# Kernel optimization log

Measured on AMD Instinct MI355X. Metric: run time of the kernel, lower is better.

The kernel has to match this reference:

```python
import jax, jax.numpy as jnp
import numpy as np

BATCH, HID, STEPS = 64, 2048, 30

def setup_inputs() -> dict:
    key = jax.random.key(0)
    ks = jax.random.split(key, 7)
    s = 1.0 / np.sqrt(HID)  # pytorch LSTM/Linear init scale
    return {
        "monthly_token": jax.random.normal(ks[0], (BATCH, HID), jnp.float32),
        "steps": STEPS,
        "W_ih": jax.random.uniform(ks[1], (4 * HID, HID), jnp.float32, -s, s),
        "W_hh": jax.random.uniform(ks[2], (4 * HID, HID), jnp.float32, -s, s),
        "b_ih": jax.random.uniform(ks[3], (4 * HID,), jnp.float32, -s, s),
        "b_hh": jax.random.uniform(ks[4], (4 * HID,), jnp.float32, -s, s),
        "W_out": jax.random.uniform(ks[5], (1, HID), jnp.float32, -s, s),
        "b_out": jax.random.uniform(ks[6], (1,), jnp.float32, -s, s),
    }

def reference(monthly_token, steps, W_ih, W_hh, b_ih, b_hh, W_out, b_out):
    H = monthly_token.shape[1]
    h0 = monthly_token                      # (B, H) initial hidden
    c0 = jnp.zeros_like(h0)
    x0 = jnp.zeros_like(h0)                 # first lstm input is zeros

    def step(carry, _):
        h, c, x = carry
        # PyTorch gate order: input, forget, cell(g), output
        gates = x @ W_ih.T + b_ih + h @ W_hh.T + b_hh   # (B, 4H)
        i, f, g, o = jnp.split(gates, 4, axis=-1)
        i = jax.nn.sigmoid(i)
        f = jax.nn.sigmoid(f)
        g = jnp.tanh(g)
        o = jax.nn.sigmoid(o)
        c_new = f * c + i * g
        h_new = o * jnp.tanh(c_new)
        y = h_new @ W_out.T + b_out          # (B, 1) daily value
        # feedback: next input is the lstm output (= h_new for 1-layer LSTM)
        return (h_new, c_new, h_new), y[:, 0]

    _, ys = jax.lax.scan(step, (h0, c0, x0), xs=None, length=steps)
    return ys.T                               # (B, steps)
```

## Files before the change

kernel.cpp:

```cpp
#include <hip/hip_runtime.h>
#include <cmath>


#define HID   2048
#define BATCH 64
#define G4    8192
#define NCU   256
#define HGRP  (HID * BATCH / 8)

typedef __attribute__((ext_vector_type(8))) _Float16 half8;
typedef __attribute__((ext_vector_type(4))) float f32x4;

#define LDS_BYTES 160768

__global__ void k_init(const float* __restrict__ token, const float* __restrict__ bih,
                       const float* __restrict__ bhh, half8* __restrict__ h0p,
                       float* __restrict__ bsum, unsigned* __restrict__ flags) {
    int g = blockIdx.x * 256 + threadIdx.x;
    int l = g & 63, nt = (g >> 6) & 3, kt = g >> 8;
    int n = nt * 16 + (l & 15);
    int k0 = kt * 32 + (l >> 4) * 8;
    const float4* ps = (const float4*)(token + (size_t)n * HID + k0);
    float4 a = ps[0], b = ps[1];
    half8 v;
    v[0]=(_Float16)a.x; v[1]=(_Float16)a.y; v[2]=(_Float16)a.z; v[3]=(_Float16)a.w;
    v[4]=(_Float16)b.x; v[5]=(_Float16)b.y; v[6]=(_Float16)b.z; v[7]=(_Float16)b.w;
    h0p[g] = v;
    if (g < G4) bsum[g] = bih[g] + bhh[g];
    if (g < NCU) flags[g] = 0u;
}

__global__ __launch_bounds__(512, 2)
void k_lstm(const float* __restrict__ wih, const float* __restrict__ whh,
            const float* __restrict__ bsum, const float* __restrict__ wout,
            _Float16* __restrict__ hbuf,
            float* __restrict__ ypart,
            unsigned* __restrict__ flags, int steps) {
    extern __shared__ char smem[];
    half8*     Wlds   = (half8*)smem;
    float*     gates  = (float*)(smem + 131072);
    f32x4*     red4   = (f32x4*)(smem + 139264);
    float*     cbuf   = (float*)(smem + 155648);
    float*     ybuf   = (float*)(smem + 157696);
    _Float16*  hstage = (_Float16*)(smem + 159744);

    const int tid  = threadIdx.x;
    const int blk  = blockIdx.x;
    const int lane = tid & 63;
    const int w    = tid >> 6;
    const int half = w & 1;
    const int ks   = w >> 1;

    for (int idx = tid; idx < 2 * 64 * 64; idx += 512) {
        int l = idx & 63, kt = (idx >> 6) & 63, m2 = idx >> 12;
        int m = l & 15;
        int gate = m2 * 2 + (m >> 3);
        int row  = gate * HID + blk * 8 + (m & 7);
        int col  = kt * 32 + (l >> 4) * 8;
        const float4* p = (const float4*)(whh + (size_t)row * HID + col);
        float4 a = p[0], b = p[1];
        half8 v;
        v[0]=(_Float16)a.x; v[1]=(_Float16)a.y; v[2]=(_Float16)a.z; v[3]=(_Float16)a.w;
        v[4]=(_Float16)b.x; v[5]=(_Float16)b.y; v[6]=(_Float16)b.z; v[7]=(_Float16)b.w;
        Wlds[idx] = v;
    }
    cbuf[tid] = 0.0f;

    float bias_r[2][4];
    if (ks == 0) {
        const int q = lane >> 4;
        #pragma unroll
        for (int mt2 = 0; mt2 < 2; ++mt2)
            #pragma unroll
            for (int r = 0; r < 4; ++r) {
                int m16 = q * 4 + r;
                bias_r[mt2][r] = bsum[(mt2 * 2 + (m16 >> 3)) * HID + blk * 8 + (m16 & 7)];
            }
    }
    const float wj = wout[blk * 8 + w];
    __syncthreads();

    for (int t = 0; t < steps; ++t) {
        const half8* hp = (const half8*)(hbuf + (size_t)t * HID * BATCH);
        f32x4 a00 = {0,0,0,0}, a01 = {0,0,0,0}, a10 = {0,0,0,0}, a11 = {0,0,0,0};
        const int ktb = ks * 16;
        #pragma unroll
        for (int kk = 0; kk < 16; ++kk) {
            int kt = ktb + kk;
            half8 av0 = Wlds[(kt) * 64 + lane];
            half8 av1 = Wlds[(64 + kt) * 64 + lane];
            half8 b0  = hp[(kt * 4 + half * 2 + 0) * 64 + lane];
            half8 b1  = hp[(kt * 4 + half * 2 + 1) * 64 + lane];
            a00 = __builtin_amdgcn_mfma_f32_16x16x32_f16(av0, b0, a00, 0, 0, 0);
            a01 = __builtin_amdgcn_mfma_f32_16x16x32_f16(av0, b1, a01, 0, 0, 0);
            a10 = __builtin_amdgcn_mfma_f32_16x16x32_f16(av1, b0, a10, 0, 0, 0);
            a11 = __builtin_amdgcn_mfma_f32_16x16x32_f16(av1, b1, a11, 0, 0, 0);
        }
        if (ks == 1 || ks == 3) {
            int srow = (ks == 3 ? 2 : 0) + half;
            red4[(srow * 4 + 0) * 64 + lane] = a00;
            red4[(srow * 4 + 1) * 64 + lane] = a01;
            red4[(srow * 4 + 2) * 64 + lane] = a10;
            red4[(srow * 4 + 3) * 64 + lane] = a11;
        }
        __syncthreads();
        if (ks == 0 || ks == 2) {
            int srow = (ks == 2 ? 2 : 0) + half;
            a00 += red4[(srow * 4 + 0) * 64 + lane];
            a01 += red4[(srow * 4 + 1) * 64 + lane];
            a10 += red4[(srow * 4 + 2) * 64 + lane];
            a11 += red4[(srow * 4 + 3) * 64 + lane];
        }
        __syncthreads();
        if (ks == 2) {
            red4[(half * 4 + 0) * 64 + lane] = a00;
            red4[(half * 4 + 1) * 64 + lane] = a01;
            red4[(half * 4 + 2) * 64 + lane] = a10;
            red4[(half * 4 + 3) * 64 + lane] = a11;
        }
        __syncthreads();
        if (ks == 0) {
            a00 += red4[(half * 4 + 0) * 64 + lane];
            a01 += red4[(half * 4 + 1) * 64 + lane];
            a10 += red4[(half * 4 + 2) * 64 + lane];
            a11 += red4[(half * 4 + 3) * 64 + lane];
            const int q = lane >> 4, col = lane & 15;
            #pragma unroll
            for (int r = 0; r < 4; ++r) {
                float* g0 = gates + (q * 4 + r) * 64 + (half * 2) * 16 + col;
                float* g1 = gates + (16 + q * 4 + r) * 64 + (half * 2) * 16 + col;
                g0[0]  = a00[r] + bias_r[0][r];
                g0[16] = a01[r] + bias_r[0][r];
                g1[0]  = a10[r] + bias_r[1][r];
                g1[16] = a11[r] + bias_r[1][r];
            }
        }
        __syncthreads();
        {
            const int b = lane;
            float gi = gates[(0  + w) * 64 + b];
            float gf = gates[(8  + w) * 64 + b];
            float gg = gates[(16 + w) * 64 + b];
            float go = gates[(24 + w) * 64 + b];
            float iv = 1.0f / (1.0f + __expf(-gi));
            float fv = 1.0f / (1.0f + __expf(-gf));
            float gv = tanhf(gg);
            float ov = 1.0f / (1.0f + __expf(-go));
            float cn = fv * cbuf[w * 64 + b] + iv * gv;
            cbuf[w * 64 + b] = cn;
            float hv = ov * tanhf(cn);
            hstage[b * 8 + w] = (_Float16)hv;
            ybuf[w * 64 + b]  = hv * wj;
        }
        __syncthreads();
        if (w == 0) {
            const int b = lane;
            const int kt = blk >> 2, quad = blk & 3;
            const int nt = b >> 4, lp = quad * 16 + (b & 15);
            const size_t g = (size_t)(kt * 4 + nt) * 64 + lp;
            unsigned long long* dst = (unsigned long long*)
                (hbuf + (size_t)(t + 1) * HID * BATCH + g * 8);
            const unsigned long long* src =
                (const unsigned long long*)(hstage + b * 8);
            unsigned long long v0 = src[0], v1 = src[1];
            __hip_atomic_store(dst,     v0, __ATOMIC_RELAXED, __HIP_MEMORY_SCOPE_AGENT);
            __hip_atomic_store(dst + 1, v1, __ATOMIC_RELAXED, __HIP_MEMORY_SCOPE_AGENT);
            asm volatile("s_waitcnt vmcnt(0)" ::: "memory");
            if (lane == 0 && t < steps - 1)
                __hip_atomic_store(&flags[blk], (unsigned)(t + 1),
                                   __ATOMIC_RELAXED, __HIP_MEMORY_SCOPE_AGENT);
            float s = ybuf[lane];
            #pragma unroll
            for (int u = 1; u < 8; ++u) s += ybuf[u * 64 + lane];
            ypart[((size_t)t * NCU + blk) * 64 + lane] = s;
        }
        if (t == 0) {
            for (int idx = tid; idx < 2 * 64 * 64; idx += 512) {
                int l = idx & 63, kt = (idx >> 6) & 63, m2 = idx >> 12;
                int m = l & 15;
                int gate = m2 * 2 + (m >> 3);
                int row  = gate * HID + blk * 8 + (m & 7);
                int col  = kt * 32 + (l >> 4) * 8;
                const float4* p = (const float4*)(wih + (size_t)row * HID + col);
                float4 a = p[0], b = p[1];
                half8 v = Wlds[idx];
                v[0] = (_Float16)((float)v[0] + a.x); v[1] = (_Float16)((float)v[1] + a.y);
                v[2] = (_Float16)((float)v[2] + a.z); v[3] = (_Float16)((float)v[3] + a.w);
                v[4] = (_Float16)((float)v[4] + b.x); v[5] = (_Float16)((float)v[5] + b.y);
                v[6] = (_Float16)((float)v[6] + b.z); v[7] = (_Float16)((float)v[7] + b.w);
                Wlds[idx] = v;
            }
            __syncthreads();
        }
        if (t < steps - 1) {
            while (__hip_atomic_load(&flags[ks * 64 + lane], __ATOMIC_RELAXED,
                                     __HIP_MEMORY_SCOPE_AGENT) <= (unsigned)t)
                __builtin_amdgcn_s_sleep(1);
            asm volatile("" ::: "memory");
        }
    }
}

__global__ __launch_bounds__(512)
void k_yout(const float* __restrict__ ypart, const float* __restrict__ bout,
            float* __restrict__ out, int steps) {
    __shared__ float red[8][64];
    int t = blockIdx.x;
    int tid = threadIdx.x;
    int b = tid & 63, ch = tid >> 6;
    const float* p = ypart + (size_t)t * NCU * 64 + b;
    float s = 0.0f;
    #pragma unroll 8
    for (int cu = ch * 32; cu < ch * 32 + 32; ++cu) s += p[(size_t)cu * 64];
    red[ch][b] = s;
    __syncthreads();
    if (tid < 64) {
        float r = bout[0];
        #pragma unroll
        for (int u = 0; u < 8; ++u) r += red[u][tid];
        out[(size_t)tid * steps + t] = r;
    }
}

extern "C" void kernel_launch(void* const* d_in, const int* in_sizes, int n_in,
                              void* d_out, int out_size, void* d_ws, size_t ws_size,
                              hipStream_t stream) {
    const float* token = (const float*)d_in[0];
    const float* wih   = (const float*)d_in[2];
    const float* whh   = (const float*)d_in[3];
    const float* bih   = (const float*)d_in[4];
    const float* bhh   = (const float*)d_in[5];
    const float* wout  = (const float*)d_in[6];
    const float* bout  = (const float*)d_in[7];
    float* out = (float*)d_out;
    const int steps = out_size / BATCH;

    char* ws = (char*)d_ws;
    size_t off = 0;
    auto carve = [&](size_t bytes) -> void* {
        void* p = ws + off;
        off = (off + bytes + 255) & ~(size_t)255;
        return p;
    };
    _Float16* hbuf  = (_Float16*)carve((size_t)(steps + 1) * HID * BATCH * 2);
    float*    bsum  = (float*)carve((size_t)G4 * 4);
    float*    ypart = (float*)carve((size_t)steps * NCU * 64 * 4);
    unsigned* flags = (unsigned*)carve(NCU * 4);

    hipFuncSetAttribute(reinterpret_cast<const void*>(&k_lstm),
                        hipFuncAttributeMaxDynamicSharedMemorySize, LDS_BYTES);

    k_init<<<dim3(HGRP / 256), dim3(256), 0, stream>>>(
        token, bih, bhh, (half8*)hbuf, bsum, flags);

    k_lstm<<<dim3(NCU), dim3(512), LDS_BYTES, stream>>>(
        wih, whh, bsum, wout, hbuf, ypart, flags, steps);

    k_yout<<<dim3(steps), dim3(512), 0, stream>>>(ypart, bout, out, steps);
}
```

Measured before the change: 439.7 us.

## Split K across all eight waves and reduce gates with LDS atomics

Each wave now owns a K slice of 8 tiles and computes all four batch column tiles, instead of a 2x4 split that needed a three-barrier tree reduction. The partial sums are combined with float atomicAdd into a double-buffered, padded LDS gate buffer that is pre-seeded with bias, which removes two barriers per step. The wait on the grid-wide flag moves to the top of the step and is spread across all waves, cell state lives in registers, and tanh is computed from exp. The cost is 32 LDS atomics per lane per step and a different floating-point summation order.

```diff
diff --git a/kernel.cpp b/kernel.cpp
--- a/kernel.cpp
+++ b/kernel.cpp
@@ -7,11 +7,13 @@
 #define G4    8192
 #define NCU   256
 #define HGRP  (HID * BATCH / 8)
+#define GSTR  68
+#define GWORDS (32 * GSTR)
 
 typedef __attribute__((ext_vector_type(8))) _Float16 half8;
 typedef __attribute__((ext_vector_type(4))) float f32x4;
 
-#define LDS_BYTES 160768
+#define LDS_BYTES 151552
 
 __global__ void k_init(const float* __restrict__ token, const float* __restrict__ bih,
                        const float* __restrict__ bhh, half8* __restrict__ h0p,
@@ -38,18 +40,14 @@
             unsigned* __restrict__ flags, int steps) {
     extern __shared__ char smem[];
     half8*     Wlds   = (half8*)smem;
-    float*     gates  = (float*)(smem + 131072);
-    f32x4*     red4   = (f32x4*)(smem + 139264);
-    float*     cbuf   = (float*)(smem + 155648);
-    float*     ybuf   = (float*)(smem + 157696);
-    _Float16*  hstage = (_Float16*)(smem + 159744);
+    float*     gbuf   = (float*)(smem + 131072);
+    _Float16*  hstage = (_Float16*)(smem + 148480);
+    float*     ybuf   = (float*)(smem + 149504);
 
     const int tid  = threadIdx.x;
     const int blk  = blockIdx.x;
     const int lane = tid & 63;
     const int w    = tid >> 6;
-    const int half = w & 1;
-    const int ks   = w >> 1;
 
     for (int idx = tid; idx < 2 * 64 * 64; idx += 512) {
         int l = idx & 63, kt = (idx >> 6) & 63, m2 = idx >> 12;
@@ -64,111 +62,117 @@
         v[4]=(_Float16)b.x; v[5]=(_Float16)b.y; v[6]=(_Float16)b.z; v[7]=(_Float16)b.w;
         Wlds[idx] = v;
     }
-    cbuf[tid] = 0.0f;
-
-    float bias_r[2][4];
-    if (ks == 0) {
-        const int q = lane >> 4;
+
+    #pragma unroll
+    for (int j = 0; j < 4; ++j) {
+        int li  = tid + j * 512;
+        int row = li >> 6;
+        int mt = row >> 4, m16 = row & 15;
+        int gate = mt * 2 + (m16 >> 3);
+        gbuf[row * GSTR + (li & 63)] = bsum[gate * HID + blk * 8 + (m16 & 7)];
+    }
+
+    const float wj = wout[blk * 8 + w];
+    float creg = 0.0f;
+
+    float bvr[5]; int bar[5];
+    if (w > 0) {
+        int idx = tid - 64;
         #pragma unroll
-        for (int mt2 = 0; mt2 < 2; ++mt2)
-            #pragma unroll
-            for (int r = 0; r < 4; ++r) {
-                int m16 = q * 4 + r;
-                bias_r[mt2][r] = bsum[(mt2 * 2 + (m16 >> 3)) * HID + blk * 8 + (m16 & 7)];
-            }
-    }
-    const float wj = wout[blk * 8 + w];
+        for (int j = 0; j < 5; ++j) {
+            int li  = idx + j * 448;
+            int row = (li >> 6) & 31;
+            int mt = row >> 4, m16 = row & 15;
+            int gate = mt * 2 + (m16 >> 3);
+            bar[j] = (li < 2048) ? (row * GSTR + (li & 63)) : -1;
+            bvr[j] = (li < 2048) ? bsum[gate * HID + blk * 8 + (m16 & 7)] : 0.0f;
+        }
+    }
     __syncthreads();
 
     for (int t = 0; t < steps; ++t) {
+        if (t) {
+            while (__hip_atomic_load(&flags[w * 32 + (lane & 31)], __ATOMIC_RELAXED,
+                                     __HIP_MEMORY_SCOPE_AGENT) < (unsigned)t)
+                __builtin_amdgcn_s_sleep(1);
+            asm volatile("" ::: "memory");
+        }
         const half8* hp = (const half8*)(hbuf + (size_t)t * HID * BATCH);
-        f32x4 a00 = {0,0,0,0}, a01 = {0,0,0,0}, a10 = {0,0,0,0}, a11 = {0,0,0,0};
-        const int ktb = ks * 16;
+        f32x4 a0[4] = {{0,0,0,0},{0,0,0,0},{0,0,0,0},{0,0,0,0}};
+        f32x4 a1[4] = {{0,0,0,0},{0,0,0,0},{0,0,0,0},{0,0,0,0}};
         #pragma unroll
-        for (int kk = 0; kk < 16; ++kk) {
-            int kt = ktb + kk;
+        for (int kk = 0; kk < 8; ++kk) {
+            const int kt = w * 8 + kk;
             half8 av0 = Wlds[(kt) * 64 + lane];
             half8 av1 = Wlds[(64 + kt) * 64 + lane];
-            half8 b0  = hp[(kt * 4 + half * 2 + 0) * 64 + lane];
-            half8 b1  = hp[(kt * 4 + half * 2 + 1) * 64 + lane];
-            a00 = __builtin_amdgcn_mfma_f32_16x16x32_f16(av0, b0, a00, 0, 0, 0);
-            a01 = __builtin_amdgcn_mfma_f32_16x16x32_f16(av0, b1, a01, 0, 0, 0);
-            a10 = __builtin_amdgcn_mfma_f32_16x16x32_f16(av1, b0, a10, 0, 0, 0);
-            a11 = __builtin_amdgcn_mfma_f32_16x16x32_f16(av1, b1, a11, 0, 0, 0);
-        }
-        if (ks == 1 || ks == 3) {
-            int srow = (ks == 3 ? 2 : 0) + half;
-            red4[(srow * 4 + 0) * 64 + lane] = a00;
-            red4[(srow * 4 + 1) * 64 + lane] = a01;
-            red4[(srow * 4 + 2) * 64 + lane] = a10;
-            red4[(srow * 4 + 3) * 64 + lane] = a11;
-        }
-        __syncthreads();
-        if (ks == 0 || ks == 2) {
-            int srow = (ks == 2 ? 2 : 0) + half;
-            a00 += red4[(srow * 4 + 0) * 64 + lane];
-            a01 += red4[(srow * 4 + 1) * 64 + lane];
-            a10 += red4[(srow * 4 + 2) * 64 + lane];
-            a11 += red4[(srow * 4 + 3) * 64 + lane];
-        }
-        __syncthreads();
-        if (ks == 2) {
-            red4[(half * 4 + 0) * 64 + lane] = a00;
-            red4[(half * 4 + 1) * 64 + lane] = a01;
-            red4[(half * 4 + 2) * 64 + lane] = a10;
-            red4[(half * 4 + 3) * 64 + lane] = a11;
-        }
-        __syncthreads();
-        if (ks == 0) {
-            a00 += red4[(half * 4 + 0) * 64 + lane];
-            a01 += red4[(half * 4 + 1) * 64 + lane];
-            a10 += red4[(half * 4 + 2) * 64 + lane];
-            a11 += red4[(half * 4 + 3) * 64 + lane];
-            const int q = lane >> 4, col = lane & 15;
+            half8 b0  = hp[(kt * 4 + 0) * 64 + lane];
+            half8 b1  = hp[(kt * 4 + 1) * 64 + lane];
+            half8 b2  = hp[(kt * 4 + 2) * 64 + lane];
+            half8 b3  = hp[(kt * 4 + 3) * 64 + lane];
+            a0[0] = __builtin_amdgcn_mfma_f32_16x16x32_f16(av0, b0, a0[0], 0, 0, 0);
+            a0[1] = __builtin_amdgcn_mfma_f32_16x16x32_f16(av0, b1, a0[1], 0, 0, 0);
+            a0[2] = __builtin_amdgcn_mfma_f32_16x16x32_f16(av0, b2, a0[2], 0, 0, 0);
+            a0[3] = __builtin_amdgcn_mfma_f32_16x16x32_f16(av0, b3, a0[3], 0, 0, 0);
+            a1[0] = __builtin_amdgcn_mfma_f32_16x16x32_f16(av1, b0, a1[0], 0, 0, 0);
+            a1[1] = __builtin_amdgcn_mfma_f32_16x16x32_f16(av1, b1, a1[1], 0, 0, 0);
+            a1[2] = __builtin_amdgcn_mfma_f32_16x16x32_f16(av1, b2, a1[2], 0, 0, 0);
+            a1[3] = __builtin_amdgcn_mfma_f32_16x16x32_f16(av1, b3, a1[3], 0, 0, 0);
+        }
+        float* Gc = gbuf + (t & 1) * GWORDS;
+        {
+            const int q4 = (lane >> 4) * 4, c16 = lane & 15;
             #pragma unroll
-            for (int r = 0; r < 4; ++r) {
-                float* g0 = gates + (q * 4 + r) * 64 + (half * 2) * 16 + col;
-                float* g1 = gates + (16 + q * 4 + r) * 64 + (half * 2) * 16 + col;
-                g0[0]  = a00[r] + bias_r[0][r];
-                g0[16] = a01[r] + bias_r[0][r];
-                g1[0]  = a10[r] + bias_r[1][r];
-                g1[16] = a11[r] + bias_r[1][r];
+            for (int nt = 0; nt < 4; ++nt) {
+                #pragma unroll
+                for (int r = 0; r < 4; ++r) {
+                    atomicAdd(&Gc[(q4 + r) * GSTR + nt * 16 + c16],      a0[nt][r]);
+                    atomicAdd(&Gc[(16 + q4 + r) * GSTR + nt * 16 + c16], a1[nt][r]);
+                }
             }
         }
         __syncthreads();
         {
-            const int b = lane;
-            float gi = gates[(0  + w) * 64 + b];
-            float gf = gates[(8  + w) * 64 + b];
-            float gg = gates[(16 + w) * 64 + b];
-            float go = gates[(24 + w) * 64 + b];
+            float gi = Gc[( 0 + w) * GSTR + lane];
+            float gf = Gc[( 8 + w) * GSTR + lane];
+            float gg = Gc[(16 + w) * GSTR + lane];
+            float go = Gc[(24 + w) * GSTR + lane];
             float iv = 1.0f / (1.0f + __expf(-gi));
             float fv = 1.0f / (1.0f + __expf(-gf));
-            float gv = tanhf(gg);
+            float eg = __expf(2.0f * gg);
+            float gv = 1.0f - 2.0f / (eg + 1.0f);
             float ov = 1.0f / (1.0f + __expf(-go));
-            float cn = fv * cbuf[w * 64 + b] + iv * gv;
-            cbuf[w * 64 + b] = cn;
-            float hv = ov * tanhf(cn);
-            hstage[b * 8 + w] = (_Float16)hv;
-            ybuf[w * 64 + b]  = hv * wj;
+            creg = fv * creg + iv * gv;
+            float ec = __expf(2.0f * creg);
+            float th = 1.0f - 2.0f / (ec + 1.0f);
+            float hv = ov * th;
+            hstage[lane * 8 + w] = (_Float16)hv;
+            ybuf[w * 64 + lane]  = hv * wj;
+        }
+        if (w > 0 && t < steps - 1) {
+            float* GN = gbuf + ((t + 1) & 1) * GWORDS;
+            #pragma unroll
+            for (int j = 0; j < 5; ++j)
+                if (bar[j] >= 0) GN[bar[j]] = bvr[j];
         }
         __syncthreads();
         if (w == 0) {
             const int b = lane;
-            const int kt = blk >> 2, quad = blk & 3;
-            const int nt = b >> 4, lp = quad * 16 + (b & 15);
-            const size_t g = (size_t)(kt * 4 + nt) * 64 + lp;
-            unsigned long long* dst = (unsigned long long*)
-                (hbuf + (size_t)(t + 1) * HID * BATCH + g * 8);
-            const unsigned long long* src =
-                (const unsigned long long*)(hstage + b * 8);
-            unsigned long long v0 = src[0], v1 = src[1];
-            __hip_atomic_store(dst,     v0, __ATOMIC_RELAXED, __HIP_MEMORY_SCOPE_AGENT);
-            __hip_atomic_store(dst + 1, v1, __ATOMIC_RELAXED, __HIP_MEMORY_SCOPE_AGENT);
-            asm volatile("s_waitcnt vmcnt(0)" ::: "memory");
-            if (lane == 0 && t < steps - 1)
-                __hip_atomic_store(&flags[blk], (unsigned)(t + 1),
-                                   __ATOMIC_RELAXED, __HIP_MEMORY_SCOPE_AGENT);
+            if (t < steps - 1) {
+                const int kt2 = blk >> 2, quad = blk & 3;
+                const int nt2 = b >> 4, lp = quad * 16 + (b & 15);
+                const size_t g = (size_t)(kt2 * 4 + nt2) * 64 + lp;
+                unsigned long long* dst = (unsigned long long*)
+                    (hbuf + (size_t)(t + 1) * HID * BATCH + g * 8);
+                const unsigned long long* src =
+                    (const unsigned long long*)(hstage + b * 8);
+                unsigned long long v0 = src[0], v1 = src[1];
+                __hip_atomic_store(dst,     v0, __ATOMIC_RELAXED, __HIP_MEMORY_SCOPE_AGENT);
+                __hip_atomic_store(dst + 1, v1, __ATOMIC_RELAXED, __HIP_MEMORY_SCOPE_AGENT);
+                asm volatile("s_waitcnt vmcnt(0)" ::: "memory");
+                if (lane == 0)
+                    __hip_atomic_store(&flags[blk], (unsigned)(t + 1),
+                                       __ATOMIC_RELAXED, __HIP_MEMORY_SCOPE_AGENT);
+            }
             float s = ybuf[lane];
             #pragma unroll
             for (int u = 1; u < 8; ++u) s += ybuf[u * 64 + lane];
@@ -191,12 +195,6 @@
                 Wlds[idx] = v;
             }
             __syncthreads();
-        }
-        if (t < steps - 1) {
-            while (__hip_atomic_load(&flags[ks * 64 + lane], __ATOMIC_RELAXED,
-                                     __HIP_MEMORY_SCOPE_AGENT) <= (unsigned)t)
-                __builtin_amdgcn_s_sleep(1);
-            asm volatile("" ::: "memory");
         }
     }
 }
```

After: 978.0 us. 2.22x slower.
